# Kernel optimization log

Hardware: AMD Instinct MI355X
Metric: run time of the kernel (lower is better)

Reference implementation:

```python
import jax, jax.numpy as jnp
import numpy as np

B, H, L, D = 8, 16, 1024, 64


def setup_inputs() -> dict:
    key = jax.random.key(0)
    kq, kk, kv, kb, km = jax.random.split(key, 5)
    q = jax.random.normal(kq, (B, H, L, D), dtype=jnp.float32)
    k = jax.random.normal(kk, (B, H, L, D), dtype=jnp.float32)
    v = jax.random.normal(kv, (B, H, L, D), dtype=jnp.float32)
    # relative-position bias, broadcast over batch
    bias = jax.random.normal(kb, (1, H, L, L), dtype=jnp.float32)
    # variable-length padding mask: each sequence has length in [L//2, L]
    lengths = jax.random.randint(km, (B,), L // 2, L + 1)
    mask = jnp.arange(L)[None, :] < lengths[:, None]  # [B, L] bool
    return {"q": q, "k": k, "v": v, "mask": mask, "bias": bias}


def reference(q, k, v, mask, bias):
    # dots: [b h m n]; NOTE: source computes self.scale but never applies it
    dots = jnp.einsum('bhmd,bhnd->bhmn', q, k) + bias
    # mask[:, None, None, :] & mask[:, None, :, None]
    m2 = mask[:, None, None, :] & mask[:, None, :, None]  # [b 1 m n]
    neg = jnp.finfo(dots.dtype).min
    probs = jax.nn.softmax(jnp.where(m2, dots, neg), axis=-1)
    probs = jnp.where(m2, probs, jnp.zeros((), dtype=probs.dtype))  # XSoftmax zeroing
    # dropout is identity in eval mode
    context = jnp.einsum('bhmn,bhnd->bhmd', probs, v)
    b, h, m, d = context.shape
    return context.transpose(0, 2, 1, 3).reshape(b, m, h * d)  # [b m (h d)]
```

## Files before the change

kernel.cpp:

```cpp
#include <hip/hip_runtime.h>
#include <hip/hip_bf16.h>

#define B_ 8
#define H_ 16
#define L_ 1024
#define D_ 64

typedef __attribute__((ext_vector_type(8))) short short8;
typedef __attribute__((ext_vector_type(4))) short short4v;
typedef __attribute__((ext_vector_type(4))) float floatx4;

__device__ inline short bf16s(float f) {
    union { float f; unsigned u; } un; un.f = f;
    unsigned u = un.u;
    u += 0x7FFFu + ((u >> 16) & 1u);
    return (short)(u >> 16);
}
__device__ inline float bf16f(unsigned short u) {
    union { unsigned u; float f; } un; un.u = ((unsigned)u) << 16;
    return un.f;
}

__device__ inline floatx4 mfma16(short8 a, short8 b, floatx4 c) {
    return __builtin_amdgcn_mfma_f32_16x16x32_bf16(a, b, c, 0, 0, 0);
}

#define KSTR 72
#define VSTR 40
#define PSTR 40
#define KPL (32 * KSTR)
#define VPL (64 * VSTR)
#define PPL (16 * PSTR)

__launch_bounds__(256, 4)
__global__ void prep_kernel(const float* __restrict__ k,
                            const float* __restrict__ v,
                            unsigned short* __restrict__ khi,
                            unsigned short* __restrict__ klo,
                            unsigned short* __restrict__ vth) {
    __shared__ alignas(16) short vt[64 * 72];
    const int bid = blockIdx.x;
    const int kt  = bid & 15;
    const int h   = (bid >> 4) & 15;
    const int b   = bid >> 8;
    const int tid = threadIdx.x;
    const size_t base = ((size_t)(b * H_ + h) * L_ + kt * 64) * D_;

    #pragma unroll
    for (int i = 0; i < 4; i++) {
        const int idx = (i * 256 + tid) * 4;
        const float4 f = *(const float4*)(k + base + idx);
        short4v hi, lo;
        hi[0] = bf16s(f.x); lo[0] = bf16s(f.x - bf16f((unsigned short)hi[0]));
        hi[1] = bf16s(f.y); lo[1] = bf16s(f.y - bf16f((unsigned short)hi[1]));
        hi[2] = bf16s(f.z); lo[2] = bf16s(f.z - bf16f((unsigned short)hi[2]));
        hi[3] = bf16s(f.w); lo[3] = bf16s(f.w - bf16f((unsigned short)hi[3]));
        *(short4v*)(khi + base + idx) = hi;
        *(short4v*)(klo + base + idx) = lo;
    }

    #pragma unroll
    for (int i = 0; i < 4; i++) {
        const int idx = (i * 256 + tid) * 4;
        const int key = idx >> 6;
        const int d0  = idx & 63;
        const float4 f = *(const float4*)(v + base + idx);
        vt[(d0 + 0) * 72 + key] = bf16s(f.x);
        vt[(d0 + 1) * 72 + key] = bf16s(f.y);
        vt[(d0 + 2) * 72 + key] = bf16s(f.z);
        vt[(d0 + 3) * 72 + key] = bf16s(f.w);
    }
    __syncthreads();
    #pragma unroll
    for (int i = 0; i < 2; i++) {
        const int s = i * 2048 + tid * 8;
        const int d = s >> 6;
        const int kk = s & 63;
        short8 r = *(const short8*)&vt[d * 72 + kk];
        *(short8*)(vth + ((size_t)((b * H_ + h) * D_) + d) * L_ + kt * 64 + kk) = r;
    }
}

__launch_bounds__(256, 4)
__global__ void attn_fast(const float* __restrict__ q,
                          const unsigned short* __restrict__ khi,
                          const unsigned short* __restrict__ klo,
                          const unsigned short* __restrict__ vth,
                          const void* __restrict__ mask,
                          const float* __restrict__ bias,
                          float* __restrict__ out) {
    __shared__ alignas(16) short lds_k[2 * 2 * KPL];
    __shared__ alignas(16) short lds_vt[2 * VPL];
    __shared__ alignas(16) short lds_p[4 * PPL];
    __shared__ int s_len;

    const int bid  = blockIdx.x;
    const int b    = (bid >> 3) & 7;
    const int p_   = ((bid >> 6) << 3) | (bid & 7);
    const int h    = p_ >> 4;
    const int mt   = p_ & 15;
    const int tid  = threadIdx.x;
    const int wave = tid >> 6;
    const int lane = tid & 63;
    const int l16  = lane & 15;
    const int quad = lane >> 4;
    short* lds_pw = lds_p + wave * PPL;

    if (tid == 0) s_len = 0;
    __syncthreads();
    {
        const unsigned char* mb = (const unsigned char*)mask;
        int fmt;
        if (mb[0] == 1 && mb[1] != 0)      fmt = 0;
        else if (mb[0] == 1)               fmt = 1;
        else if (mb[1] != 0)               fmt = 2;
        else                               fmt = 1;
        int s = 0;
        if (fmt == 0) {
            const unsigned char* r = mb + b * L_;
            #pragma unroll
            for (int i = 0; i < 4; i++) s += (r[tid * 4 + i] != 0);
        } else if (fmt == 1) {
            const unsigned int* r = (const unsigned int*)mask + b * L_;
            #pragma unroll
            for (int i = 0; i < 4; i++) s += (r[tid * 4 + i] != 0u);
        } else {
            const unsigned short* r = (const unsigned short*)mask + b * L_;
            #pragma unroll
            for (int i = 0; i < 4; i++) s += (r[tid * 4 + i] != 0);
        }
        #pragma unroll
        for (int off = 32; off; off >>= 1) s += __shfl_down(s, off);
        if (lane == 0) atomicAdd(&s_len, s);
    }
    __syncthreads();
    const int len = s_len;

    const int m_base = mt * 64 + wave * 16;
    const float* qp = q + ((size_t)((b * H_ + h) * L_) + (m_base + l16)) * D_;
    short8 qh[2], ql[2];
    #pragma unroll
    for (int c = 0; c < 2; c++)
        #pragma unroll
        for (int j = 0; j < 8; j++) {
            float x = qp[c * 32 + quad * 8 + j];
            short hh = bf16s(x);
            qh[c][j] = hh;
            ql[c][j] = bf16s(x - bf16f((unsigned short)hh));
        }

    floatx4 acc[4];
    float l_p[4];
    #pragma unroll
    for (int c = 0; c < 4; c++) { acc[c][0] = acc[c][1] = acc[c][2] = acc[c][3] = 0.f; }
    #pragma unroll
    for (int r = 0; r < 4; r++) l_p[r] = 0.f;

    const size_t kvoff = (size_t)((b * H_ + h) * L_) * D_;
    const size_t vtoff = (size_t)((b * H_ + h) * D_) * L_;
    const float* bias_base = bias + (size_t)h * L_ * L_
                           + (size_t)(m_base + quad * 4) * L_ + l16;

    const int ntiles = (len + 31) >> 5;

    const int key_s = tid >> 3;
    const int d_s   = (tid & 7) * 8;
    const int dv    = tid >> 2;
    const int k8v   = (tid & 3) * 8;

    short8 kh_r, kl_r, vv_r;
    float bc[8], bn[8];

    {
        const size_t ksrc = kvoff + (size_t)tid * 8;
        kh_r = *(const short8*)(khi + ksrc);
        kl_r = *(const short8*)(klo + ksrc);
        vv_r = *(const short8*)(vth + vtoff + (size_t)dv * L_ + k8v);
        #pragma unroll
        for (int r = 0; r < 4; r++) {
            bc[2 * r]     = bias_base[(size_t)r * L_];
            bc[2 * r + 1] = bias_base[(size_t)r * L_ + 16];
        }
        *(short8*)&lds_k[key_s * KSTR + d_s] = kh_r;
        *(short8*)&lds_k[KPL + key_s * KSTR + d_s] = kl_r;
        *(short8*)&lds_vt[dv * VSTR + k8v] = vv_r;
    }
    __syncthreads();

    for (int kt = 0; kt < ntiles; kt++) {
        const int n0 = kt * 32;
        short* kb = lds_k + (kt & 1) * (2 * KPL);
        short* vb = lds_vt + (kt & 1) * VPL;
        const bool pfetch = (kt + 1 < ntiles);

        if (pfetch) {
            const size_t ksrc = kvoff + (size_t)(n0 + 32) * D_ + (size_t)tid * 8;
            kh_r = *(const short8*)(khi + ksrc);
            kl_r = *(const short8*)(klo + ksrc);
            vv_r = *(const short8*)(vth + vtoff + (size_t)dv * L_ + (n0 + 32) + k8v);
            #pragma unroll
            for (int r = 0; r < 4; r++) {
                bn[2 * r]     = bias_base[(size_t)r * L_ + n0 + 32];
                bn[2 * r + 1] = bias_base[(size_t)r * L_ + n0 + 48];
            }
        }

        floatx4 s0, s1;
        s0[0]=s0[1]=s0[2]=s0[3]=0.f;
        s1[0]=s1[1]=s1[2]=s1[3]=0.f;
        __builtin_amdgcn_s_setprio(1);
        #pragma unroll
        for (int c = 0; c < 2; c++) {
            const int o0 = l16 * KSTR + c * 32 + quad * 8;
            const int o1 = (16 + l16) * KSTR + c * 32 + quad * 8;
            short8 k0h = *(const short8*)&kb[o0];
            short8 k1h = *(const short8*)&kb[o1];
            short8 k0l = *(const short8*)&kb[KPL + o0];
            short8 k1l = *(const short8*)&kb[KPL + o1];
            s0 = mfma16(qh[c], k0h, s0);
            s0 = mfma16(ql[c], k0h, s0);
            s0 = mfma16(qh[c], k0l, s0);
            s1 = mfma16(qh[c], k1h, s1);
            s1 = mfma16(ql[c], k1h, s1);
            s1 = mfma16(qh[c], k1l, s1);
        }
        __builtin_amdgcn_s_setprio(0);

        #pragma unroll
        for (int r = 0; r < 4; r++) { s0[r] += bc[2 * r]; s1[r] += bc[2 * r + 1]; }
        if (n0 + l16      >= len) { s0[0]=s0[1]=s0[2]=s0[3] = -1e30f; }
        if (n0 + 16 + l16 >= len) { s1[0]=s1[1]=s1[2]=s1[3] = -1e30f; }

        #pragma unroll
        for (int r = 0; r < 4; r++) {
            const float p0 = __expf(fminf(s0[r], 60.f));
            const float p1 = __expf(fminf(s1[r], 60.f));
            l_p[r] += p0 + p1;
            const int row = quad * 4 + r;
            lds_pw[row * PSTR + l16]      = bf16s(p0);
            lds_pw[row * PSTR + 16 + l16] = bf16s(p1);
        }

        short8 pfr = *(const short8*)&lds_pw[l16 * PSTR + quad * 8];
        __builtin_amdgcn_s_setprio(1);
        #pragma unroll
        for (int c = 0; c < 4; c++) {
            short8 vf = *(const short8*)&vb[(c * 16 + l16) * VSTR + quad * 8];
            acc[c] = mfma16(pfr, vf, acc[c]);
        }
        __builtin_amdgcn_s_setprio(0);

        if (pfetch) {
            short* kb2 = lds_k + ((kt + 1) & 1) * (2 * KPL);
            short* vb2 = lds_vt + ((kt + 1) & 1) * VPL;
            *(short8*)&kb2[key_s * KSTR + d_s] = kh_r;
            *(short8*)&kb2[KPL + key_s * KSTR + d_s] = kl_r;
            *(short8*)&vb2[dv * VSTR + k8v] = vv_r;
            #pragma unroll
            for (int i = 0; i < 8; i++) bc[i] = bn[i];
        }
        __syncthreads();
    }

    #pragma unroll
    for (int r = 0; r < 4; r++) {
        float ls = l_p[r];
        #pragma unroll
        for (int off = 8; off; off >>= 1) ls += __shfl_xor(ls, off);
        const int mg = m_base + quad * 4 + r;
        const bool valid = (mg < len);
        const float invl = (ls > 0.f) ? (1.0f / ls) : 0.f;
        float* op = out + (size_t)(b * L_ + mg) * (H_ * D_) + h * D_;
        #pragma unroll
        for (int c = 0; c < 4; c++)
            op[c * 16 + l16] = valid ? acc[c][r] * invl : 0.f;
    }
}

__launch_bounds__(256, 4)
__global__ void attn_fallback(const float* __restrict__ q,
                              const float* __restrict__ k,
                              const float* __restrict__ v,
                              const void* __restrict__ mask,
                              const float* __restrict__ bias,
                              float* __restrict__ out) {
    __shared__ alignas(16) short lds_k[2 * KPL];
    __shared__ alignas(16) short lds_vt[2 * VPL];
    __shared__ alignas(16) short lds_p[4 * 2 * PPL];
    __shared__ int s_len;

    const int bid  = blockIdx.x;
    const int mt   = bid & 15;
    const int h    = (bid >> 4) & 15;
    const int b    = bid >> 8;
    const int tid  = threadIdx.x;
    const int wave = tid >> 6;
    const int lane = tid & 63;
    const int l16  = lane & 15;
    const int quad = lane >> 4;
    short* lds_pw = lds_p + wave * (2 * PPL);

    if (tid == 0) s_len = 0;
    __syncthreads();
    {
        const unsigned char* mb = (const unsigned char*)mask;
        int fmt;
        if (mb[0] == 1 && mb[1] != 0)      fmt = 0;
        else if (mb[0] == 1)               fmt = 1;
        else if (mb[1] != 0)               fmt = 2;
        else                               fmt = 1;
        int s = 0;
        if (fmt == 0) {
            const unsigned char* r = mb + b * L_;
            for (int i = 0; i < 4; i++) s += (r[tid * 4 + i] != 0);
        } else if (fmt == 1) {
            const unsigned int* r = (const unsigned int*)mask + b * L_;
            for (int i = 0; i < 4; i++) s += (r[tid * 4 + i] != 0u);
        } else {
            const unsigned short* r = (const unsigned short*)mask + b * L_;
            for (int i = 0; i < 4; i++) s += (r[tid * 4 + i] != 0);
        }
        for (int off = 32; off; off >>= 1) s += __shfl_down(s, off);
        if (lane == 0) atomicAdd(&s_len, s);
    }
    __syncthreads();
    const int len = s_len;

    const int m_base = mt * 64 + wave * 16;
    const float* qp = q + ((size_t)((b * H_ + h) * L_) + (m_base + l16)) * D_;
    short8 qh[2], ql[2];
    for (int c = 0; c < 2; c++)
        for (int j = 0; j < 8; j++) {
            float x = qp[c * 32 + quad * 8 + j];
            short hh = bf16s(x);
            qh[c][j] = hh;
            ql[c][j] = bf16s(x - bf16f((unsigned short)hh));
        }

    floatx4 acc[4];
    float m_i[4], l_i[4];
    for (int c = 0; c < 4; c++) { acc[c][0]=acc[c][1]=acc[c][2]=acc[c][3]=0.f; }
    for (int r = 0; r < 4; r++) { m_i[r] = -1e30f; l_i[r] = 0.f; }

    const size_t kvoff = (size_t)((b * H_ + h) * L_) * D_;
    const size_t boff0 = (size_t)h * L_ * L_;
    const int ntiles = (len + 31) >> 5;

    for (int kt = 0; kt < ntiles; kt++) {
        const int n0 = kt * 32;
        __syncthreads();
        {
            const int e0  = tid * 8;
            const int key = e0 >> 6;
            const int d0  = e0 & 63;
            const float* ksrc = k + kvoff + (size_t)(n0 + key) * D_ + d0;
            const float* vsrc = v + kvoff + (size_t)(n0 + key) * D_ + d0;
            short* kdh = &lds_k[key * KSTR + d0];
            for (int i = 0; i < 8; i++) {
                float x = ksrc[i];
                short hh = bf16s(x);
                kdh[i]       = hh;
                kdh[KPL + i] = bf16s(x - bf16f((unsigned short)hh));
            }
            for (int i = 0; i < 8; i++) {
                float x = vsrc[i];
                short hh = bf16s(x);
                lds_vt[(d0 + i) * VSTR + key]       = hh;
                lds_vt[VPL + (d0 + i) * VSTR + key] = bf16s(x - bf16f((unsigned short)hh));
            }
        }
        __syncthreads();

        floatx4 s0, s1;
        s0[0]=s0[1]=s0[2]=s0[3]=0.f;
        s1[0]=s1[1]=s1[2]=s1[3]=0.f;
        for (int c = 0; c < 2; c++) {
            const int o0 = l16 * KSTR + c * 32 + quad * 8;
            const int o1 = (16 + l16) * KSTR + c * 32 + quad * 8;
            short8 k0h = *(const short8*)&lds_k[o0];
            short8 k1h = *(const short8*)&lds_k[o1];
            short8 k0l = *(const short8*)&lds_k[KPL + o0];
            short8 k1l = *(const short8*)&lds_k[KPL + o1];
            s0 = mfma16(qh[c], k0h, s0);
            s0 = mfma16(ql[c], k0h, s0);
            s0 = mfma16(qh[c], k0l, s0);
            s1 = mfma16(qh[c], k1h, s1);
            s1 = mfma16(ql[c], k1h, s1);
            s1 = mfma16(qh[c], k1l, s1);
        }

        for (int r = 0; r < 4; r++) {
            const float* bp = bias + boff0 + (size_t)(m_base + quad * 4 + r) * L_ + n0;
            s0[r] += bp[l16];
            s1[r] += bp[16 + l16];
        }
        if (n0 + l16      >= len) { s0[0]=s0[1]=s0[2]=s0[3] = -1e30f; }
        if (n0 + 16 + l16 >= len) { s1[0]=s1[1]=s1[2]=s1[3] = -1e30f; }

        for (int r = 0; r < 4; r++) {
            float mx = fmaxf(s0[r], s1[r]);
            for (int off = 8; off; off >>= 1) mx = fmaxf(mx, __shfl_xor(mx, off));
            const float mnew  = fmaxf(m_i[r], mx);
            const float alpha = __expf(m_i[r] - mnew);
            const float p0 = __expf(s0[r] - mnew);
            const float p1 = __expf(s1[r] - mnew);
            float ps = p0 + p1;
            for (int off = 8; off; off >>= 1) ps += __shfl_xor(ps, off);
            l_i[r] = l_i[r] * alpha + ps;
            m_i[r] = mnew;
            for (int c = 0; c < 4; c++) acc[c][r] *= alpha;
            const int row = quad * 4 + r;
            short h0 = bf16s(p0), h1 = bf16s(p1);
            lds_pw[row * PSTR + l16]      = h0;
            lds_pw[row * PSTR + 16 + l16] = h1;
            lds_pw[PPL + row * PSTR + l16]      = bf16s(p0 - bf16f((unsigned short)h0));
            lds_pw[PPL + row * PSTR + 16 + l16] = bf16s(p1 - bf16f((unsigned short)h1));
        }

        short8 pfh = *(const short8*)&lds_pw[l16 * PSTR + quad * 8];
        short8 pfl = *(const short8*)&lds_pw[PPL + l16 * PSTR + quad * 8];
        for (int c = 0; c < 4; c++) {
            const int vo = (c * 16 + l16) * VSTR + quad * 8;
            short8 vfh = *(const short8*)&lds_vt[vo];
            short8 vfl = *(const short8*)&lds_vt[VPL + vo];
            acc[c] = mfma16(pfh, vfh, acc[c]);
            acc[c] = mfma16(pfl, vfh, acc[c]);
            acc[c] = mfma16(pfh, vfl, acc[c]);
        }
    }

    for (int r = 0; r < 4; r++) {
        const int mg = m_base + quad * 4 + r;
        const bool valid = (mg < len);
        const float invl = (l_i[r] > 0.f) ? (1.0f / l_i[r]) : 0.f;
        float* op = out + (size_t)(b * L_ + mg) * (H_ * D_) + h * D_;
        for (int c = 0; c < 4; c++)
            op[c * 16 + l16] = valid ? acc[c][r] * invl : 0.f;
    }
}

extern "C" void kernel_launch(void* const* d_in, const int* in_sizes, int n_in,
                              void* d_out, int out_size, void* d_ws, size_t ws_size,
                              hipStream_t stream) {
    const float* q    = (const float*)d_in[0];
    const float* k    = (const float*)d_in[1];
    const float* v    = (const float*)d_in[2];
    const void*  mask = d_in[3];
    const float* bias = (const float*)d_in[4];
    float* out = (float*)d_out;

    const size_t PLANE = (size_t)B_ * H_ * L_ * D_;
    const size_t need  = 3 * PLANE * sizeof(unsigned short);

    dim3 grid(B_ * H_ * (L_ / 64));
    if (ws_size >= need) {
        unsigned short* khi = (unsigned short*)d_ws;
        unsigned short* klo = khi + PLANE;
        unsigned short* vth = klo + PLANE;
        prep_kernel<<<grid, 256, 0, stream>>>(k, v, khi, klo, vth);
        attn_fast<<<grid, 256, 0, stream>>>(q, khi, klo, vth, mask, bias, out);
    } else {
        attn_fallback<<<grid, 256, 0, stream>>>(q, k, v, mask, bias, out);
    }
}
```

Measured before the change: 277.1 us.

## Use 512-thread blocks covering 128 query rows with split K/V loaders

Each attention block now covers 128 query rows with 8 waves instead of 64 rows with 4 waves, halving the number of blocks. The K and V tiles staged in LDS are shared by twice as many waves, so each key/value tile is fetched from global memory half as often. Threads are split so the first half loads K hi/lo and the second half loads V, cutting per-thread prefetch registers. Launch bounds change to 512 threads with 6 blocks per CU, and the grid shrinks to 1024 blocks, which may hurt load balance and occupancy.

```diff
diff --git a/kernel.cpp b/kernel.cpp
--- a/kernel.cpp
+++ b/kernel.cpp
@@ -81,7 +81,7 @@
     }
 }
 
-__launch_bounds__(256, 4)
+__launch_bounds__(512, 6)
 __global__ void attn_fast(const float* __restrict__ q,
                           const unsigned short* __restrict__ khi,
                           const unsigned short* __restrict__ klo,
@@ -91,14 +91,14 @@
                           float* __restrict__ out) {
     __shared__ alignas(16) short lds_k[2 * 2 * KPL];
     __shared__ alignas(16) short lds_vt[2 * VPL];
-    __shared__ alignas(16) short lds_p[4 * PPL];
+    __shared__ alignas(16) short lds_p[8 * PPL];
     __shared__ int s_len;
 
     const int bid  = blockIdx.x;
     const int b    = (bid >> 3) & 7;
     const int p_   = ((bid >> 6) << 3) | (bid & 7);
-    const int h    = p_ >> 4;
-    const int mt   = p_ & 15;
+    const int h    = p_ >> 3;
+    const int mt2  = p_ & 7;
     const int tid  = threadIdx.x;
     const int wave = tid >> 6;
     const int lane = tid & 63;
@@ -108,7 +108,7 @@
 
     if (tid == 0) s_len = 0;
     __syncthreads();
-    {
+    if (tid < 256) {
         const unsigned char* mb = (const unsigned char*)mask;
         int fmt;
         if (mb[0] == 1 && mb[1] != 0)      fmt = 0;
@@ -136,7 +136,7 @@
     __syncthreads();
     const int len = s_len;
 
-    const int m_base = mt * 64 + wave * 16;
+    const int m_base = mt2 * 128 + wave * 16;
     const float* qp = q + ((size_t)((b * H_ + h) * L_) + (m_base + l16)) * D_;
     short8 qh[2], ql[2];
     #pragma unroll
@@ -163,27 +163,32 @@
 
     const int ntiles = (len + 31) >> 5;
 
-    const int key_s = tid >> 3;
-    const int d_s   = (tid & 7) * 8;
-    const int dv    = tid >> 2;
-    const int k8v   = (tid & 3) * 8;
+    const bool isK  = (tid < 256);
+    const int  t8   = tid & 255;
+    const int  key_s = t8 >> 3;
+    const int  d_s   = (t8 & 7) * 8;
+    const int  dv    = t8 >> 2;
+    const int  k8v   = (t8 & 3) * 8;
 
     short8 kh_r, kl_r, vv_r;
     float bc[8], bn[8];
 
     {
-        const size_t ksrc = kvoff + (size_t)tid * 8;
-        kh_r = *(const short8*)(khi + ksrc);
-        kl_r = *(const short8*)(klo + ksrc);
-        vv_r = *(const short8*)(vth + vtoff + (size_t)dv * L_ + k8v);
+        if (isK) {
+            const size_t ksrc = kvoff + (size_t)t8 * 8;
+            kh_r = *(const short8*)(khi + ksrc);
+            kl_r = *(const short8*)(klo + ksrc);
+            *(short8*)&lds_k[key_s * KSTR + d_s] = kh_r;
+            *(short8*)&lds_k[KPL + key_s * KSTR + d_s] = kl_r;
+        } else {
+            vv_r = *(const short8*)(vth + vtoff + (size_t)dv * L_ + k8v);
+            *(short8*)&lds_vt[dv * VSTR + k8v] = vv_r;
+        }
         #pragma unroll
         for (int r = 0; r < 4; r++) {
             bc[2 * r]     = bias_base[(size_t)r * L_];
             bc[2 * r + 1] = bias_base[(size_t)r * L_ + 16];
         }
-        *(short8*)&lds_k[key_s * KSTR + d_s] = kh_r;
-        *(short8*)&lds_k[KPL + key_s * KSTR + d_s] = kl_r;
-        *(short8*)&lds_vt[dv * VSTR + k8v] = vv_r;
     }
     __syncthreads();
 
@@ -194,10 +199,13 @@
         const bool pfetch = (kt + 1 < ntiles);
 
         if (pfetch) {
-            const size_t ksrc = kvoff + (size_t)(n0 + 32) * D_ + (size_t)tid * 8;
-            kh_r = *(const short8*)(khi + ksrc);
-            kl_r = *(const short8*)(klo + ksrc);
-            vv_r = *(const short8*)(vth + vtoff + (size_t)dv * L_ + (n0 + 32) + k8v);
+            if (isK) {
+                const size_t ksrc = kvoff + (size_t)(n0 + 32) * D_ + (size_t)t8 * 8;
+                kh_r = *(const short8*)(khi + ksrc);
+                kl_r = *(const short8*)(klo + ksrc);
+            } else {
+                vv_r = *(const short8*)(vth + vtoff + (size_t)dv * L_ + (n0 + 32) + k8v);
+            }
             #pragma unroll
             for (int r = 0; r < 4; r++) {
                 bn[2 * r]     = bias_base[(size_t)r * L_ + n0 + 32];
@@ -253,9 +261,12 @@
         if (pfetch) {
             short* kb2 = lds_k + ((kt + 1) & 1) * (2 * KPL);
             short* vb2 = lds_vt + ((kt + 1) & 1) * VPL;
-            *(short8*)&kb2[key_s * KSTR + d_s] = kh_r;
-            *(short8*)&kb2[KPL + key_s * KSTR + d_s] = kl_r;
-            *(short8*)&vb2[dv * VSTR + k8v] = vv_r;
+            if (isK) {
+                *(short8*)&kb2[key_s * KSTR + d_s] = kh_r;
+                *(short8*)&kb2[KPL + key_s * KSTR + d_s] = kl_r;
+            } else {
+                *(short8*)&vb2[dv * VSTR + k8v] = vv_r;
+            }
             #pragma unroll
             for (int i = 0; i < 8; i++) bc[i] = bn[i];
         }
@@ -452,14 +463,13 @@
     const size_t PLANE = (size_t)B_ * H_ * L_ * D_;
     const size_t need  = 3 * PLANE * sizeof(unsigned short);
 
-    dim3 grid(B_ * H_ * (L_ / 64));
     if (ws_size >= need) {
         unsigned short* khi = (unsigned short*)d_ws;
         unsigned short* klo = khi + PLANE;
         unsigned short* vth = klo + PLANE;
-        prep_kernel<<<grid, 256, 0, stream>>>(k, v, khi, klo, vth);
-        attn_fast<<<grid, 256, 0, stream>>>(q, khi, klo, vth, mask, bias, out);
+        prep_kernel<<<dim3(B_ * H_ * (L_ / 64)), 256, 0, stream>>>(k, v, khi, klo, vth);
+        attn_fast<<<dim3(B_ * H_ * (L_ / 128)), 512, 0, stream>>>(q, khi, klo, vth, mask, bias, out);
     } else {
-        attn_fallback<<<grid, 256, 0, stream>>>(q, k, v, mask, bias, out);
-    }
-}
+        attn_fallback<<<dim3(B_ * H_ * (L_ / 64)), 256, 0, stream>>>(q, k, v, mask, bias, out);
+    }
+}
```

After: 452.9 us. +63.4%, slower.

## Process two 16-row query sub-tiles per wave to reuse K/V LDS tiles

Applied to the files above, without the earlier changes.

Each wave now handles 32 query rows as two 16-row sub-tiles, so the block covers 128 rows and the grid is halved. Each K and V fragment read from LDS feeds twice as many MFMAs, and each block streams the K/V tiles for twice as many rows, which cuts LDS and global K/V traffic per output row. The bias loads are no longer register-prefetched one tile ahead; they are issued inside each iteration. In exchange the kernel uses more registers and a larger P scratch buffer, drops the occupancy hint from 4 to 3 waves, and launches half as many blocks, which risks underfilling the GPU.

```diff
diff --git a/kernel.cpp b/kernel.cpp
--- a/kernel.cpp
+++ b/kernel.cpp
@@ -81,7 +81,7 @@
     }
 }
 
-__launch_bounds__(256, 4)
+__launch_bounds__(256, 3)
 __global__ void attn_fast(const float* __restrict__ q,
                           const unsigned short* __restrict__ khi,
                           const unsigned short* __restrict__ klo,
@@ -91,20 +91,20 @@
                           float* __restrict__ out) {
     __shared__ alignas(16) short lds_k[2 * 2 * KPL];
     __shared__ alignas(16) short lds_vt[2 * VPL];
-    __shared__ alignas(16) short lds_p[4 * PPL];
+    __shared__ alignas(16) short lds_p[4 * 2 * PPL];
     __shared__ int s_len;
 
     const int bid  = blockIdx.x;
     const int b    = (bid >> 3) & 7;
     const int p_   = ((bid >> 6) << 3) | (bid & 7);
-    const int h    = p_ >> 4;
-    const int mt   = p_ & 15;
+    const int h    = p_ >> 3;
+    const int mt2  = p_ & 7;
     const int tid  = threadIdx.x;
     const int wave = tid >> 6;
     const int lane = tid & 63;
     const int l16  = lane & 15;
     const int quad = lane >> 4;
-    short* lds_pw = lds_p + wave * PPL;
+    short* lds_pw = lds_p + wave * (2 * PPL);
 
     if (tid == 0) s_len = 0;
     __syncthreads();
@@ -136,25 +136,33 @@
     __syncthreads();
     const int len = s_len;
 
-    const int m_base = mt * 64 + wave * 16;
-    const float* qp = q + ((size_t)((b * H_ + h) * L_) + (m_base + l16)) * D_;
-    short8 qh[2], ql[2];
+    const int m_base = mt2 * 128 + wave * 32;
+    const float* qp0 = q + ((size_t)((b * H_ + h) * L_) + (m_base + l16)) * D_;
+    const float* qp1 = qp0 + (size_t)16 * D_;
+    short8 qh0[2], ql0[2], qh1[2], ql1[2];
     #pragma unroll
     for (int c = 0; c < 2; c++)
         #pragma unroll
         for (int j = 0; j < 8; j++) {
-            float x = qp[c * 32 + quad * 8 + j];
-            short hh = bf16s(x);
-            qh[c][j] = hh;
-            ql[c][j] = bf16s(x - bf16f((unsigned short)hh));
-        }
-
-    floatx4 acc[4];
-    float l_p[4];
-    #pragma unroll
-    for (int c = 0; c < 4; c++) { acc[c][0] = acc[c][1] = acc[c][2] = acc[c][3] = 0.f; }
-    #pragma unroll
-    for (int r = 0; r < 4; r++) l_p[r] = 0.f;
+            float x0 = qp0[c * 32 + quad * 8 + j];
+            short h0 = bf16s(x0);
+            qh0[c][j] = h0;
+            ql0[c][j] = bf16s(x0 - bf16f((unsigned short)h0));
+            float x1 = qp1[c * 32 + quad * 8 + j];
+            short h1 = bf16s(x1);
+            qh1[c][j] = h1;
+            ql1[c][j] = bf16s(x1 - bf16f((unsigned short)h1));
+        }
+
+    floatx4 acc0[4], acc1[4];
+    float l_p0[4], l_p1[4];
+    #pragma unroll
+    for (int c = 0; c < 4; c++) {
+        acc0[c][0]=acc0[c][1]=acc0[c][2]=acc0[c][3]=0.f;
+        acc1[c][0]=acc1[c][1]=acc1[c][2]=acc1[c][3]=0.f;
+    }
+    #pragma unroll
+    for (int r = 0; r < 4; r++) { l_p0[r] = 0.f; l_p1[r] = 0.f; }
 
     const size_t kvoff = (size_t)((b * H_ + h) * L_) * D_;
     const size_t vtoff = (size_t)((b * H_ + h) * D_) * L_;
@@ -169,18 +177,12 @@
     const int k8v   = (tid & 3) * 8;
 
     short8 kh_r, kl_r, vv_r;
-    float bc[8], bn[8];
 
     {
         const size_t ksrc = kvoff + (size_t)tid * 8;
         kh_r = *(const short8*)(khi + ksrc);
         kl_r = *(const short8*)(klo + ksrc);
         vv_r = *(const short8*)(vth + vtoff + (size_t)dv * L_ + k8v);
-        #pragma unroll
-        for (int r = 0; r < 4; r++) {
-            bc[2 * r]     = bias_base[(size_t)r * L_];
-            bc[2 * r + 1] = bias_base[(size_t)r * L_ + 16];
-        }
         *(short8*)&lds_k[key_s * KSTR + d_s] = kh_r;
         *(short8*)&lds_k[KPL + key_s * KSTR + d_s] = kl_r;
         *(short8*)&lds_vt[dv * VSTR + k8v] = vv_r;
@@ -198,16 +200,22 @@
             kh_r = *(const short8*)(khi + ksrc);
             kl_r = *(const short8*)(klo + ksrc);
             vv_r = *(const short8*)(vth + vtoff + (size_t)dv * L_ + (n0 + 32) + k8v);
-            #pragma unroll
-            for (int r = 0; r < 4; r++) {
-                bn[2 * r]     = bias_base[(size_t)r * L_ + n0 + 32];
-                bn[2 * r + 1] = bias_base[(size_t)r * L_ + n0 + 48];
-            }
-        }
-
-        floatx4 s0, s1;
-        s0[0]=s0[1]=s0[2]=s0[3]=0.f;
-        s1[0]=s1[1]=s1[2]=s1[3]=0.f;
+        }
+
+        float bc[16];
+        #pragma unroll
+        for (int r = 0; r < 4; r++) {
+            bc[2 * r]          = bias_base[(size_t)r * L_ + n0];
+            bc[2 * r + 1]      = bias_base[(size_t)r * L_ + n0 + 16];
+            bc[8 + 2 * r]      = bias_base[(size_t)(16 + r) * L_ + n0];
+            bc[8 + 2 * r + 1]  = bias_base[(size_t)(16 + r) * L_ + n0 + 16];
+        }
+
+        floatx4 s0a, s1a, s0b, s1b;
+        s0a[0]=s0a[1]=s0a[2]=s0a[3]=0.f;
+        s1a[0]=s1a[1]=s1a[2]=s1a[3]=0.f;
+        s0b[0]=s0b[1]=s0b[2]=s0b[3]=0.f;
+        s1b[0]=s1b[1]=s1b[2]=s1b[3]=0.f;
         __builtin_amdgcn_s_setprio(1);
         #pragma unroll
         for (int c = 0; c < 2; c++) {
@@ -217,36 +225,58 @@
             short8 k1h = *(const short8*)&kb[o1];
             short8 k0l = *(const short8*)&kb[KPL + o0];
             short8 k1l = *(const short8*)&kb[KPL + o1];
-            s0 = mfma16(qh[c], k0h, s0);
-            s0 = mfma16(ql[c], k0h, s0);
-            s0 = mfma16(qh[c], k0l, s0);
-            s1 = mfma16(qh[c], k1h, s1);
-            s1 = mfma16(ql[c], k1h, s1);
-            s1 = mfma16(qh[c], k1l, s1);
+            s0a = mfma16(qh0[c], k0h, s0a);
+            s0a = mfma16(ql0[c], k0h, s0a);
+            s0a = mfma16(qh0[c], k0l, s0a);
+            s1a = mfma16(qh0[c], k1h, s1a);
+            s1a = mfma16(ql0[c], k1h, s1a);
+            s1a = mfma16(qh0[c], k1l, s1a);
+            s0b = mfma16(qh1[c], k0h, s0b);
+            s0b = mfma16(ql1[c], k0h, s0b);
+            s0b = mfma16(qh1[c], k0l, s0b);
+            s1b = mfma16(qh1[c], k1h, s1b);
+            s1b = mfma16(ql1[c], k1h, s1b);
+            s1b = mfma16(qh1[c], k1l, s1b);
         }
         __builtin_amdgcn_s_setprio(0);
 
         #pragma unroll
-        for (int r = 0; r < 4; r++) { s0[r] += bc[2 * r]; s1[r] += bc[2 * r + 1]; }
-        if (n0 + l16      >= len) { s0[0]=s0[1]=s0[2]=s0[3] = -1e30f; }
-        if (n0 + 16 + l16 >= len) { s1[0]=s1[1]=s1[2]=s1[3] = -1e30f; }
-
-        #pragma unroll
         for (int r = 0; r < 4; r++) {
-            const float p0 = __expf(fminf(s0[r], 60.f));
-            const float p1 = __expf(fminf(s1[r], 60.f));
-            l_p[r] += p0 + p1;
+            s0a[r] += bc[2 * r];     s1a[r] += bc[2 * r + 1];
+            s0b[r] += bc[8 + 2 * r]; s1b[r] += bc[8 + 2 * r + 1];
+        }
+        if (n0 + l16 >= len) {
+            s0a[0]=s0a[1]=s0a[2]=s0a[3] = -1e30f;
+            s0b[0]=s0b[1]=s0b[2]=s0b[3] = -1e30f;
+        }
+        if (n0 + 16 + l16 >= len) {
+            s1a[0]=s1a[1]=s1a[2]=s1a[3] = -1e30f;
+            s1b[0]=s1b[1]=s1b[2]=s1b[3] = -1e30f;
+        }
+
+        #pragma unroll
+        for (int r = 0; r < 4; r++) {
             const int row = quad * 4 + r;
-            lds_pw[row * PSTR + l16]      = bf16s(p0);
-            lds_pw[row * PSTR + 16 + l16] = bf16s(p1);
-        }
-
-        short8 pfr = *(const short8*)&lds_pw[l16 * PSTR + quad * 8];
+            const float p0a = __expf(fminf(s0a[r], 60.f));
+            const float p1a = __expf(fminf(s1a[r], 60.f));
+            l_p0[r] += p0a + p1a;
+            lds_pw[row * PSTR + l16]      = bf16s(p0a);
+            lds_pw[row * PSTR + 16 + l16] = bf16s(p1a);
+            const float p0b = __expf(fminf(s0b[r], 60.f));
+            const float p1b = __expf(fminf(s1b[r], 60.f));
+            l_p1[r] += p0b + p1b;
+            lds_pw[PPL + row * PSTR + l16]      = bf16s(p0b);
+            lds_pw[PPL + row * PSTR + 16 + l16] = bf16s(p1b);
+        }
+
+        short8 pf0 = *(const short8*)&lds_pw[l16 * PSTR + quad * 8];
+        short8 pf1 = *(const short8*)&lds_pw[PPL + l16 * PSTR + quad * 8];
         __builtin_amdgcn_s_setprio(1);
         #pragma unroll
         for (int c = 0; c < 4; c++) {
             short8 vf = *(const short8*)&vb[(c * 16 + l16) * VSTR + quad * 8];
-            acc[c] = mfma16(pfr, vf, acc[c]);
+            acc0[c] = mfma16(pf0, vf, acc0[c]);
+            acc1[c] = mfma16(pf1, vf, acc1[c]);
         }
         __builtin_amdgcn_s_setprio(0);
 
@@ -256,24 +286,32 @@
             *(short8*)&kb2[key_s * KSTR + d_s] = kh_r;
             *(short8*)&kb2[KPL + key_s * KSTR + d_s] = kl_r;
             *(short8*)&vb2[dv * VSTR + k8v] = vv_r;
-            #pragma unroll
-            for (int i = 0; i < 8; i++) bc[i] = bn[i];
         }
         __syncthreads();
     }
 
     #pragma unroll
     for (int r = 0; r < 4; r++) {
-        float ls = l_p[r];
-        #pragma unroll
-        for (int off = 8; off; off >>= 1) ls += __shfl_xor(ls, off);
-        const int mg = m_base + quad * 4 + r;
-        const bool valid = (mg < len);
-        const float invl = (ls > 0.f) ? (1.0f / ls) : 0.f;
-        float* op = out + (size_t)(b * L_ + mg) * (H_ * D_) + h * D_;
-        #pragma unroll
-        for (int c = 0; c < 4; c++)
-            op[c * 16 + l16] = valid ? acc[c][r] * invl : 0.f;
+        float ls0 = l_p0[r];
+        float ls1 = l_p1[r];
+        #pragma unroll
+        for (int off = 8; off; off >>= 1) {
+            ls0 += __shfl_xor(ls0, off);
+            ls1 += __shfl_xor(ls1, off);
+        }
+        const int mg0 = m_base + quad * 4 + r;
+        const int mg1 = mg0 + 16;
+        const bool v0 = (mg0 < len);
+        const bool v1 = (mg1 < len);
+        const float i0 = (ls0 > 0.f) ? (1.0f / ls0) : 0.f;
+        const float i1 = (ls1 > 0.f) ? (1.0f / ls1) : 0.f;
+        float* op0 = out + (size_t)(b * L_ + mg0) * (H_ * D_) + h * D_;
+        float* op1 = out + (size_t)(b * L_ + mg1) * (H_ * D_) + h * D_;
+        #pragma unroll
+        for (int c = 0; c < 4; c++) {
+            op0[c * 16 + l16] = v0 ? acc0[c][r] * i0 : 0.f;
+            op1[c * 16 + l16] = v1 ? acc1[c][r] * i1 : 0.f;
+        }
     }
 }
 
@@ -452,14 +490,13 @@
     const size_t PLANE = (size_t)B_ * H_ * L_ * D_;
     const size_t need  = 3 * PLANE * sizeof(unsigned short);
 
-    dim3 grid(B_ * H_ * (L_ / 64));
     if (ws_size >= need) {
         unsigned short* khi = (unsigned short*)d_ws;
         unsigned short* klo = khi + PLANE;
         unsigned short* vth = klo + PLANE;
-        prep_kernel<<<grid, 256, 0, stream>>>(k, v, khi, klo, vth);
-        attn_fast<<<grid, 256, 0, stream>>>(q, khi, klo, vth, mask, bias, out);
+        prep_kernel<<<dim3(B_ * H_ * (L_ / 64)), 256, 0, stream>>>(k, v, khi, klo, vth);
+        attn_fast<<<dim3(B_ * H_ * (L_ / 128)), 256, 0, stream>>>(q, khi, klo, vth, mask, bias, out);
     } else {
-        attn_fallback<<<grid, 256, 0, stream>>>(q, k, v, mask, bias, out);
-    }
-}
+        attn_fallback<<<dim3(B_ * H_ * (L_ / 64)), 256, 0, stream>>>(q, k, v, mask, bias, out);
+    }
+}
```

Result: no change. 282.3 us (+1.8%).

## Schedule attention tiles longest-batch-first via atomic work queue

Applied to the files above, without the earlier changes.

Mask lengths are now computed once in the prep kernel and stored in a small control buffer, so the attention kernel no longer recounts them in every block. The attention blocks take work items from an atomic counter and map them to batches sorted by descending sequence length. The long, expensive batches therefore start first and the short ones fill in the tail, which should reduce load imbalance at the end of the grid. The cost is one global atomic per block plus a tiny per-block sort, and the design relies on the prep kernel having finished and reset the counter before the attention kernel runs.

```diff
diff --git a/kernel.cpp b/kernel.cpp
--- a/kernel.cpp
+++ b/kernel.cpp
@@ -35,15 +35,52 @@
 __launch_bounds__(256, 4)
 __global__ void prep_kernel(const float* __restrict__ k,
                             const float* __restrict__ v,
+                            const void* __restrict__ mask,
                             unsigned short* __restrict__ khi,
                             unsigned short* __restrict__ klo,
-                            unsigned short* __restrict__ vth) {
+                            unsigned short* __restrict__ vth,
+                            int* __restrict__ qctl) {
     __shared__ alignas(16) short vt[64 * 72];
+    __shared__ int cnt;
     const int bid = blockIdx.x;
     const int kt  = bid & 15;
     const int h   = (bid >> 4) & 15;
     const int b   = bid >> 8;
     const int tid = threadIdx.x;
+
+    if (bid < 8) {
+        if (tid == 0) cnt = 0;
+        __syncthreads();
+        const unsigned char* mb = (const unsigned char*)mask;
+        int fmt;
+        if (mb[0] == 1 && mb[1] != 0)      fmt = 0;
+        else if (mb[0] == 1)               fmt = 1;
+        else if (mb[1] != 0)               fmt = 2;
+        else                               fmt = 1;
+        int s = 0;
+        if (fmt == 0) {
+            const unsigned char* r = mb + bid * L_;
+            #pragma unroll
+            for (int i = 0; i < 4; i++) s += (r[tid * 4 + i] != 0);
+        } else if (fmt == 1) {
+            const unsigned int* r = (const unsigned int*)mask + bid * L_;
+            #pragma unroll
+            for (int i = 0; i < 4; i++) s += (r[tid * 4 + i] != 0u);
+        } else {
+            const unsigned short* r = (const unsigned short*)mask + bid * L_;
+            #pragma unroll
+            for (int i = 0; i < 4; i++) s += (r[tid * 4 + i] != 0);
+        }
+        #pragma unroll
+        for (int off = 32; off; off >>= 1) s += __shfl_down(s, off);
+        if ((tid & 63) == 0) atomicAdd(&cnt, s);
+        __syncthreads();
+        if (tid == 0) {
+            qctl[1 + bid] = cnt;
+            if (bid == 0) qctl[0] = 0;
+        }
+    }
+
     const size_t base = ((size_t)(b * H_ + h) * L_ + kt * 64) * D_;
 
     #pragma unroll
@@ -86,19 +123,15 @@
                           const unsigned short* __restrict__ khi,
                           const unsigned short* __restrict__ klo,
                           const unsigned short* __restrict__ vth,
-                          const void* __restrict__ mask,
                           const float* __restrict__ bias,
-                          float* __restrict__ out) {
+                          float* __restrict__ out,
+                          int* __restrict__ qctl) {
     __shared__ alignas(16) short lds_k[2 * 2 * KPL];
     __shared__ alignas(16) short lds_vt[2 * VPL];
     __shared__ alignas(16) short lds_p[4 * PPL];
-    __shared__ int s_len;
-
-    const int bid  = blockIdx.x;
-    const int b    = (bid >> 3) & 7;
-    const int p_   = ((bid >> 6) << 3) | (bid & 7);
-    const int h    = p_ >> 4;
-    const int mt   = p_ & 15;
+    __shared__ int s_item;
+    __shared__ int s_bl;
+
     const int tid  = threadIdx.x;
     const int wave = tid >> 6;
     const int lane = tid & 63;
@@ -106,35 +139,31 @@
     const int quad = lane >> 4;
     short* lds_pw = lds_p + wave * PPL;
 
-    if (tid == 0) s_len = 0;
-    __syncthreads();
-    {
-        const unsigned char* mb = (const unsigned char*)mask;
-        int fmt;
-        if (mb[0] == 1 && mb[1] != 0)      fmt = 0;
-        else if (mb[0] == 1)               fmt = 1;
-        else if (mb[1] != 0)               fmt = 2;
-        else                               fmt = 1;
-        int s = 0;
-        if (fmt == 0) {
-            const unsigned char* r = mb + b * L_;
-            #pragma unroll
-            for (int i = 0; i < 4; i++) s += (r[tid * 4 + i] != 0);
-        } else if (fmt == 1) {
-            const unsigned int* r = (const unsigned int*)mask + b * L_;
-            #pragma unroll
-            for (int i = 0; i < 4; i++) s += (r[tid * 4 + i] != 0u);
-        } else {
-            const unsigned short* r = (const unsigned short*)mask + b * L_;
-            #pragma unroll
-            for (int i = 0; i < 4; i++) s += (r[tid * 4 + i] != 0);
-        }
-        #pragma unroll
-        for (int off = 32; off; off >>= 1) s += __shfl_down(s, off);
-        if (lane == 0) atomicAdd(&s_len, s);
-    }
-    __syncthreads();
-    const int len = s_len;
+    if (tid == 0) s_item = atomicAdd(qctl, 1);
+    __syncthreads();
+    const int idx = s_item;
+    if (tid == 0) {
+        const int* lens = qctl + 1;
+        int ls[8], ord[8];
+        #pragma unroll
+        for (int i = 0; i < 8; i++) { ls[i] = lens[i]; ord[i] = i; }
+        #pragma unroll
+        for (int i = 1; i < 8; i++) {
+            int lv = ls[i], ov = ord[i], j = i;
+            while (j > 0 && ls[j - 1] < lv) {
+                ls[j] = ls[j - 1]; ord[j] = ord[j - 1]; j--;
+            }
+            ls[j] = lv; ord[j] = ov;
+        }
+        const int rank = idx >> 8;
+        s_bl = (ord[rank] << 16) | ls[rank];
+    }
+    __syncthreads();
+    const int b   = s_bl >> 16;
+    const int len = s_bl & 0xffff;
+    const int r_  = idx & 255;
+    const int h   = r_ >> 4;
+    const int mt  = r_ & 15;
 
     const int m_base = mt * 64 + wave * 16;
     const float* qp = q + ((size_t)((b * H_ + h) * L_) + (m_base + l16)) * D_;
@@ -450,16 +479,16 @@
     float* out = (float*)d_out;
 
     const size_t PLANE = (size_t)B_ * H_ * L_ * D_;
-    const size_t need  = 3 * PLANE * sizeof(unsigned short);
-
-    dim3 grid(B_ * H_ * (L_ / 64));
+    const size_t need  = 3 * PLANE * sizeof(unsigned short) + 64;
+
     if (ws_size >= need) {
         unsigned short* khi = (unsigned short*)d_ws;
         unsigned short* klo = khi + PLANE;
         unsigned short* vth = klo + PLANE;
-        prep_kernel<<<grid, 256, 0, stream>>>(k, v, khi, klo, vth);
-        attn_fast<<<grid, 256, 0, stream>>>(q, khi, klo, vth, mask, bias, out);
+        int* qctl = (int*)(vth + PLANE);
+        prep_kernel<<<dim3(B_ * H_ * (L_ / 64)), 256, 0, stream>>>(k, v, mask, khi, klo, vth, qctl);
+        attn_fast<<<dim3(B_ * H_ * (L_ / 64)), 256, 0, stream>>>(q, khi, klo, vth, bias, out, qctl);
     } else {
-        attn_fallback<<<grid, 256, 0, stream>>>(q, k, v, mask, bias, out);
-    }
-}
+        attn_fallback<<<dim3(B_ * H_ * (L_ / 64)), 256, 0, stream>>>(q, k, v, mask, bias, out);
+    }
+}
```

Measured after the change: 285.8 us. 3.1% more time.
